# Performance work log

Hardware: AMD Instinct MI355X
Metric: run time of the kernel (lower is better)

## Reference

```python
import jax, jax.numpy as jnp
import numpy as np

H, C, PQ, PV, CZ, CS = 12, 16, 4, 8, 128, 384
W_C = (2.0 / (9.0 * PQ)) ** 0.5
INV_SQRT3 = 3.0 ** -0.5


def setup_inputs() -> dict:
    key = jax.random.key(0)
    ks = jax.random.split(key, 20)
    B, N = 2, 512
    s = jax.random.normal(ks[0], (B, N, CS), jnp.float32)
    z = jax.random.normal(ks[1], (B, N, N, CZ), jnp.float32)
    m = jax.random.normal(ks[2], (B, N, 3, 3), jnp.float32)
    rot, _ = jnp.linalg.qr(m)  # proper-ish rotations (orthonormal frames)
    trans = jax.random.normal(ks[3], (B, N, 3), jnp.float32)
    seq_mask = jnp.ones((B, N), jnp.float32)
    sc = 0.02
    params = {
        'Wq': jax.random.normal(ks[4], (CS, H * C)) * sc,
        'bq': jnp.zeros((H * C,)),
        'Wkv': jax.random.normal(ks[5], (CS, H * C * 2)) * sc,
        'bkv': jnp.zeros((H * C * 2,)),
        'Wb': jax.random.normal(ks[6], (CZ, H)) * sc,
        'bb': jnp.zeros((H,)),
        'Wqp': jax.random.normal(ks[7], (CS, 3 * PQ * H)) * sc,
        'bqp': jnp.zeros((3 * PQ * H,)),
        'Wkvp': jax.random.normal(ks[8], (CS, 3 * (PQ + PV) * H)) * sc,
        'bkvp': jnp.zeros((3 * (PQ + PV) * H,)),
        'gamma': jnp.zeros((H,)),
        'Wout': jax.random.normal(ks[9], ((CZ + C + PV * 4) * H, CS)) * sc,
        'bout': jnp.zeros((CS,)),
    }
    return dict(s=s, z=z, rot=rot, trans=trans, seq_mask=seq_mask, **params)


def reference(s, z, rot, trans, seq_mask, Wq, bq, Wkv, bkv, Wb, bb, Wqp, bqp, Wkvp, bkvp, gamma, Wout, bout):
    B, N, _ = s.shape
    # scalar q/k/v
    q = (s @ Wq + bq).reshape(B, N, H, C)
    kv = (s @ Wkv + bkv).reshape(B, N, H, 2 * C)
    k, v = kv[..., :C], kv[..., C:]
    qp = s @ Wqp + bqp                                   # (B,N,3*PQ*H)
    qp = jnp.stack(jnp.split(qp, 3, axis=-1), axis=-1)   # (B,N,PQ*H,3)
    qp = jnp.einsum('bixy,bipy->bipx', rot, qp) + trans[:, :, None, :]
    qp = qp.reshape(B, N, H, PQ, 3)
    # key/value points
    kvp = s @ Wkvp + bkvp
    kvp = jnp.stack(jnp.split(kvp, 3, axis=-1), axis=-1)  # (B,N,(PQ+PV)*H,3)
    kvp = jnp.einsum('bixy,bipy->bipx', rot, kvp) + trans[:, :, None, :]
    kvp = kvp.reshape(B, N, H, PQ + PV, 3)
    kp, vp = kvp[..., :PQ, :], kvp[..., PQ:, :]
    # attention logits: scalar term + pair bias + point-distance term
    bpair = (z @ Wb + bb).transpose(0, 3, 1, 2)          # (B,H,i,j)
    a = jnp.einsum('bihc,bjhc->bhij', q, k) * (3 * C) ** -0.5 + INV_SQRT3 * bpair
    d2 = jnp.sum((qp[:, :, None] - kp[:, None]) ** 2, axis=-1)   # (B,i,j,H,PQ)
    pa = -0.5 * jnp.sum(d2, axis=-1)                      # (B,i,j,H)
    head_w = jax.nn.softplus(gamma)
    pa = pa * (head_w * W_C * INV_SQRT3)
    a = a + pa.transpose(0, 3, 1, 2)
    mask_bias = 100000.0 * (seq_mask[:, :, None] * seq_mask[:, None, :] - 1.0)
    a = a + mask_bias[:, None, :, :]
    a = jax.nn.softmax(a, axis=-1)                        # (B,H,i,j)
    # outputs: scalar values, rotated points (inverse frame), pair features
    o = jnp.einsum('bhij,bjhc->bihc', a, v).reshape(B, N, H * C)
    op = jnp.einsum('bhij,bjhpx->bihpx', a, vp)           # (B,i,H,PV,3)
    op = jnp.einsum('biyx,bihpy->bihpx', rot, op - trans[:, :, None, None, :])  # R^T(p-t)
    onorm = jnp.maximum(jnp.sqrt(jnp.sum(op ** 2, axis=-1)), 1e-6).reshape(B, N, H * PV)
    op = op.reshape(B, N, H * PV, 3)
    opair = jnp.einsum('bhij,bijc->bihc', a, z).reshape(B, N, H * CZ)
    feat = jnp.concatenate([o, op[..., 0], op[..., 1], op[..., 2], onorm, opair], axis=-1)
    return feat @ Wout + bout
```

## Files before the change

kernel.cpp:

```cpp
#include <hip/hip_runtime.h>
#include <hip/hip_bf16.h>

constexpr int B = 2, N = 512, H = 12, C = 16, PQ = 4, PV = 8, CZ = 128, CS = 384;
constexpr int HC   = H * C;
constexpr int FEAT = (CZ + C + PV * 4) * H;
constexpr float QK_SCALE  = 0.14433756729740643f;
constexpr float INV_SQRT3 = 0.5773502691896258f;
constexpr float WC_IS3    = 0.13608276348795434f;

using f32x4 = __attribute__((ext_vector_type(4))) float;
using s16x8 = __attribute__((ext_vector_type(8))) short;

__device__ __forceinline__ short f2b(float f) {
    union { __hip_bfloat16 b; short s; } u;
    u.b = __float2bfloat16(f);
    return u.s;
}
__device__ __forceinline__ float b2f(short s) {
    union { short s; __hip_bfloat16 b; } u;
    u.s = s;
    return __bfloat162float(u.b);
}

__device__ __forceinline__ size_t kkps_idx(int row, int col) {
    return ((size_t)((row >> 4) * 12 + (col >> 5))) * 512
         + (size_t)(((row & 15) << 2) + ((col & 31) >> 3)) * 8 + (col & 7);
}

constexpr int RPB = 2;

__global__ __launch_bounds__(256) void k_proj(
    const float* __restrict__ s, const float* __restrict__ rot, const float* __restrict__ trans,
    const float* __restrict__ Wq, const float* __restrict__ bq,
    const float* __restrict__ Wkv, const float* __restrict__ bkv,
    const float* __restrict__ Wqp, const float* __restrict__ bqp,
    const float* __restrict__ Wkvp, const float* __restrict__ bkvp,
    const float* __restrict__ gamma, const float* __restrict__ bb,
    const float* __restrict__ Wout,
    short* __restrict__ qcw, short* __restrict__ kkpS,
    float* __restrict__ vw, float* __restrict__ vpw,
    short* __restrict__ pcw, float* __restrict__ auxw,
    short* __restrict__ WT)
{
    __shared__ float s_s[RPB][CS];
    __shared__ float rawqp_s[RPB][144];
    __shared__ float rawkvp_s[RPB][432];
    __shared__ float qrot_s[RPB][48][3];
    __shared__ float sq_s[RPB][48];
    __shared__ float R_s[RPB][9], T_s[RPB][3];
    const int t = threadIdx.x;
    const int bi0 = blockIdx.x * RPB;

    for (int idx = t; idx < RPB * CS / 4; idx += 256) {
        int r = idx / (CS / 4), k4 = idx % (CS / 4);
        ((float4*)s_s[r])[k4] = ((const float4*)(s + (size_t)(bi0 + r) * CS))[k4];
    }
    if (t < RPB * 9) R_s[t / 9][t % 9] = rot[bi0 * 9 + t];
    if (t < RPB * 3) T_s[t / 3][t % 3] = trans[bi0 * 3 + t];
    __syncthreads();

    for (int qd = t; qd < 288; qd += 256) {
        const int c = qd * 4;
        const float* Wp; int ldw; const float* bp;
        int seg;
        if (c < 192)      { Wp = Wq   + c;        ldw = 192; bp = bq + c;        seg = 0; }
        else if (c < 576) { Wp = Wkv  + (c - 192); ldw = 384; bp = bkv + (c - 192); seg = 1; }
        else if (c < 720) { Wp = Wqp  + (c - 576); ldw = 144; bp = bqp + (c - 576); seg = 2; }
        else              { Wp = Wkvp + (c - 720); ldw = 432; bp = bkvp + (c - 720); seg = 3; }
        float4 bv = *(const float4*)bp;
        float acc[RPB][4];
        #pragma unroll
        for (int r = 0; r < RPB; ++r) {
            acc[r][0] = bv.x; acc[r][1] = bv.y; acc[r][2] = bv.z; acc[r][3] = bv.w;
        }
        for (int k4 = 0; k4 < CS / 4; ++k4) {
            float4 sv[RPB];
            #pragma unroll
            for (int r = 0; r < RPB; ++r) sv[r] = *(const float4*)&s_s[r][k4 * 4];
            #pragma unroll
            for (int e = 0; e < 4; ++e) {
                float4 wv = *(const float4*)(Wp + (size_t)(k4 * 4 + e) * ldw);
                #pragma unroll
                for (int r = 0; r < RPB; ++r) {
                    float se = ((const float*)&sv[r])[e];
                    acc[r][0] += se * wv.x; acc[r][1] += se * wv.y;
                    acc[r][2] += se * wv.z; acc[r][3] += se * wv.w;
                }
            }
        }
        if (seg == 0) {
            #pragma unroll
            for (int r = 0; r < RPB; ++r) {
                short4 o = make_short4(f2b(QK_SCALE * acc[r][0]), f2b(QK_SCALE * acc[r][1]),
                                       f2b(QK_SCALE * acc[r][2]), f2b(QK_SCALE * acc[r][3]));
                *(short4*)&qcw[(size_t)(bi0 + r) * 192 + c] = o;
            }
        } else if (seg == 1) {
            int cc = c - 192, h = cc >> 5, w5 = cc & 31;
            if (w5 < 16) {
                int col = h * 16 + w5;
                #pragma unroll
                for (int r = 0; r < RPB; ++r) {
                    short4 o = make_short4(f2b(acc[r][0]), f2b(acc[r][1]),
                                           f2b(acc[r][2]), f2b(acc[r][3]));
                    *(short4*)&kkpS[kkps_idx(bi0 + r, col)] = o;
                }
            } else {
                #pragma unroll
                for (int r = 0; r < RPB; ++r) {
                    int row = bi0 + r;
                    *(float4*)&vw[(size_t)row * 192 + h * 16 + (w5 - 16)] =
                        (float4){acc[r][0], acc[r][1], acc[r][2], acc[r][3]};
                }
            }
        } else if (seg == 2) {
            #pragma unroll
            for (int r = 0; r < RPB; ++r)
                *(float4*)&rawqp_s[r][c - 576] = (float4){acc[r][0], acc[r][1], acc[r][2], acc[r][3]};
        } else {
            #pragma unroll
            for (int r = 0; r < RPB; ++r)
                *(float4*)&rawkvp_s[r][c - 720] = (float4){acc[r][0], acc[r][1], acc[r][2], acc[r][3]};
        }
    }
    __syncthreads();

    for (int idx = t; idx < RPB * 48; idx += 256) {
        int r = idx / 48, p = idx % 48;
        float y0 = rawqp_s[r][p], y1 = rawqp_s[r][48 + p], y2 = rawqp_s[r][96 + p];
        #pragma unroll
        for (int x = 0; x < 3; ++x)
            qrot_s[r][p][x] = T_s[r][x] + R_s[r][x * 3] * y0 + R_s[r][x * 3 + 1] * y1 + R_s[r][x * 3 + 2] * y2;
    }
    for (int idx = t; idx < RPB * 144; idx += 256) {
        int r = idx / 144, p = idx % 144, h = p / 12, pp = p % 12;
        float y0 = rawkvp_s[r][p], y1 = rawkvp_s[r][144 + p], y2 = rawkvp_s[r][288 + p];
        float vals[3]; float ss = 0.0f;
        #pragma unroll
        for (int x = 0; x < 3; ++x) {
            float v = T_s[r][x] + R_s[r][x * 3] * y0 + R_s[r][x * 3 + 1] * y1 + R_s[r][x * 3 + 2] * y2;
            vals[x] = v; ss += v * v;
        }
        int row = bi0 + r;
        if (pp < PQ) {
            #pragma unroll
            for (int x = 0; x < 3; ++x)
                kkpS[kkps_idx(row, 192 + h * 16 + pp * 3 + x)] = f2b(vals[x]);
            sq_s[r][h * 4 + pp] = ss;
        } else {
            #pragma unroll
            for (int x = 0; x < 3; ++x)
                vpw[(size_t)row * 288 + h * 24 + (pp - PQ) * 3 + x] = vals[x];
        }
    }
    __syncthreads();

    if (t < RPB * 12) {
        int r = t / 12, h = t % 12, row = bi0 + r;
        float g = gamma[h];
        float sp = fmaxf(g, 0.0f) + log1pf(expf(-fabsf(g)));
        float pac = -0.5f * sp * WC_IS3;
        float kpsq = sq_s[r][h * 4] + sq_s[r][h * 4 + 1] + sq_s[r][h * 4 + 2] + sq_s[r][h * 4 + 3];
        kkpS[kkps_idx(row, 192 + h * 16 + 12)] = f2b(kpsq);
        kkpS[kkps_idx(row, 192 + h * 16 + 13)] = 0;
        kkpS[kkps_idx(row, 192 + h * 16 + 14)] = 0;
        kkpS[kkps_idx(row, 192 + h * 16 + 15)] = 0;
        float qpsq = 0.0f;
        #pragma unroll
        for (int pq = 0; pq < 4; ++pq)
            #pragma unroll
            for (int x = 0; x < 3; ++x) {
                float qv = qrot_s[r][h * 4 + pq][x];
                qpsq += qv * qv;
                pcw[(size_t)row * 192 + h * 16 + pq * 3 + x] = f2b(-2.0f * pac * qv);
            }
        pcw[(size_t)row * 192 + h * 16 + 12] = f2b(pac);
        pcw[(size_t)row * 192 + h * 16 + 13] = 0;
        pcw[(size_t)row * 192 + h * 16 + 14] = 0;
        pcw[(size_t)row * 192 + h * 16 + 15] = 0;
        auxw[(size_t)row * 16 + h] = INV_SQRT3 * bb[h] + pac * qpsq;
    }
    if (t >= RPB * 12 && t < RPB * 16) {
        int r = (t - RPB * 12) >> 2, hh = 12 + ((t - RPB * 12) & 3);
        auxw[(size_t)(bi0 + r) * 16 + hh] = 0.0f;
    }

    short* tileb = (short*)&s_s[0][0];
    for (int tile = blockIdx.x; tile < 66 * 12; tile += 512) {
        const int k0 = (tile % 66) * 32;
        const int c0 = (tile / 66) * 32;
        __syncthreads();
        {
            int r = t >> 3, c4 = (t & 7) * 4;
            float4 v = *(const float4*)&Wout[(size_t)(k0 + r) * CS + c0 + c4];
            tileb[(c4 + 0) * 33 + r] = f2b(v.x);
            tileb[(c4 + 1) * 33 + r] = f2b(v.y);
            tileb[(c4 + 2) * 33 + r] = f2b(v.z);
            tileb[(c4 + 3) * 33 + r] = f2b(v.w);
        }
        __syncthreads();
        {
            int rr = t >> 3, k4 = (t & 7) * 4;
            short4 o = make_short4(tileb[rr * 33 + k4], tileb[rr * 33 + k4 + 1],
                                   tileb[rr * 33 + k4 + 2], tileb[rr * 33 + k4 + 3]);
            *(short4*)&WT[(size_t)(c0 + rr) * FEAT + k0 + k4] = o;
        }
    }
}

constexpr int PLS = 520;
constexpr int BSEL = 56;

#define LOADZ(BUF, PTR)                                                  \
    {                                                                    \
        _Pragma("unroll")                                                \
        for (int k4 = 0; k4 < 4; ++k4) {                                 \
            BUF[k4 * 2]     = *(const float4*)((PTR) + k4 * 32);         \
            BUF[k4 * 2 + 1] = *(const float4*)((PTR) + k4 * 32 + 4);     \
        }                                                                \
    }

#define COMPUTE(BUF, JC, KPTR)                                                     \
    {                                                                              \
        s16x8 zf[4];                                                               \
        _Pragma("unroll")                                                          \
        for (int kk = 0; kk < 4; ++kk) {                                           \
            float4 u0 = BUF[kk * 2], u1 = BUF[kk * 2 + 1];                         \
            s16x8 f;                                                               \
            f[0] = f2b(u0.x); f[1] = f2b(u0.y); f[2] = f2b(u0.z); f[3] = f2b(u0.w);\
            f[4] = f2b(u1.x); f[5] = f2b(u1.y); f[6] = f2b(u1.z); f[7] = f2b(u1.w);\
            zf[kk] = f;                                                            \
        }                                                                          \
        f32x4 accA = (f32x4){0, 0, 0, 0}, accB = (f32x4){0, 0, 0, 0};              \
        f32x4 accC = (f32x4){0, 0, 0, 0}, accD = (f32x4){0, 0, 0, 0};              \
        _Pragma("unroll")                                                          \
        for (int kk = 0; kk < 4; ++kk) {                                           \
            s16x8 wb = *(const s16x8*)(bl + kk * 8);                               \
            accA = __builtin_amdgcn_mfma_f32_16x16x32_bf16(zf[kk], wb, accA, 0, 0, 0);\
        }                                                                          \
        s16x8 qselr = *(const s16x8*)(bl + 32);                                    \
        s16x8 pselr = *(const s16x8*)(bl + 40);                                    \
        _Pragma("unroll")                                                          \
        for (int kk = 0; kk < 4; ++kk) {                                           \
            s16x8 af = *(const s16x8*)((KPTR) + kk * 512);                         \
            s16x8 bsel = (kk == half) ? qselr : z8;                                \
            accB = __builtin_amdgcn_mfma_f32_16x16x32_bf16(af, bsel, accB, 0, 0, 0); \
        }                                                                          \
        _Pragma("unroll")                                                          \
        for (int kk = 4; kk < 8; ++kk) {                                           \
            s16x8 af = *(const s16x8*)((KPTR) + kk * 512);                         \
            s16x8 bsel;                                                            \
            if (kk < 6) bsel = (kk == half) ? qselr : z8;                          \
            else        bsel = ((kk - 6) == half) ? pselr : z8;                    \
            accC = __builtin_amdgcn_mfma_f32_16x16x32_bf16(af, bsel, accC, 0, 0, 0); \
        }                                                                          \
        _Pragma("unroll")                                                          \
        for (int kk = 8; kk < 12; ++kk) {                                          \
            s16x8 af = *(const s16x8*)((KPTR) + kk * 512);                         \
            s16x8 bsel = ((kk - 6) == half) ? pselr : z8;                          \
            accD = __builtin_amdgcn_mfma_f32_16x16x32_bf16(af, bsel, accD, 0, 0, 0); \
        }                                                                          \
        f32x4 acc = (accA + accB) + (accC + accD);                                 \
        float4 m4 = *(const float4*)(mkp + (JC) * 16);                             \
        float lo[4]; float cm = -INFINITY;                                         \
        _Pragma("unroll")                                                          \
        for (int r = 0; r < 4; ++r) {                                              \
            lo[r] = acc[r] + constH + 100000.0f * (mask_i * ((const float*)&m4)[r] - 1.0f); \
            cm = fmaxf(cm, lo[r]);                                                 \
        }                                                                          \
        cm = fmaxf(cm, __shfl_xor(cm, 16, 64));                                    \
        cm = fmaxf(cm, __shfl_xor(cm, 32, 64));                                    \
        float mnew = fmaxf(m_run, cm);                                             \
        float sc = __expf(m_run - mnew);                                           \
        m_run = mnew;                                                              \
        float p[4]; float ps = 0.0f;                                               \
        _Pragma("unroll")                                                          \
        for (int r = 0; r < 4; ++r) { p[r] = __expf(lo[r] - mnew); ps += p[r]; }   \
        ps += __shfl_xor(ps, 16, 64);                                              \
        ps += __shfl_xor(ps, 32, 64);                                              \
        l_run = l_run * sc + ps;                                                   \
        if (sc != 1.0f) {                                                          \
            for (int jj = lg * 4; jj < (JC) * 16; jj += 16) {                      \
                short* pr = &P_lds[m15 * PLS + jw + jj];                           \
                _Pragma("unroll")                                                  \
                for (int r = 0; r < 4; ++r) pr[r] = f2b(b2f(pr[r]) * sc);          \
            }                                                                      \
        }                                                                          \
        *(short4*)&P_lds[m15 * PLS + jw + (JC) * 16 + lg * 4] =                    \
            make_short4(f2b(p[0]), f2b(p[1]), f2b(p[2]), f2b(p[3]));               \
    }

__global__ __launch_bounds__(256) void k_attn2(
    const float* __restrict__ z, const float* __restrict__ rot, const float* __restrict__ trans,
    const float* __restrict__ seq_mask,
    const float* __restrict__ Wb,
    const short* __restrict__ qcw, const short* __restrict__ kkpS,
    const short* __restrict__ pcw, const float* __restrict__ auxw,
    const float* __restrict__ vw, const float* __restrict__ vpw,
    short* __restrict__ featb)
{
    __shared__ short P_lds[16 * PLS];
    __shared__ __align__(16) char ovl[7680];
    short* bsel_lds = (short*)ovl;
    float* ored_s   = (float*)ovl;
    float* opred_s  = (float*)(ovl + 3072);
    float* op_f     = (float*)(ovl + 6528);
    __shared__ float ml_s[4][16], ll_s[4][16], M_s[16], Linv_s[16];
    __shared__ float R_s[9], T_s[3];

    const int t = threadIdx.x;
    const int w   = t >> 6;
    const int l   = t & 63;
    const int lg  = l >> 4;
    const int m15 = l & 15;
    const int bi  = blockIdx.x;
    const int b   = bi >> 9;
    const int i   = bi & (N - 1);

    if (t < 9) R_s[t] = rot[bi * 9 + t];
    if (t < 3) T_s[t] = trans[bi * 3 + t];

    const bool hv = (m15 < 12);
    const int hcl = hv ? m15 : 0;
    const int half = m15 >> 1;
    const float constH = auxw[(size_t)bi * 16 + m15];
    const float mask_i = seq_mask[bi];

    if (w == 0) {
        short* dst = &bsel_lds[l * BSEL];
        #pragma unroll
        for (int kk = 0; kk < 4; ++kk)
            #pragma unroll
            for (int e = 0; e < 8; ++e) {
                int c = kk * 32 + lg * 8 + e;
                dst[kk * 8 + e] = f2b(hv ? INV_SQRT3 * Wb[c * H + hcl] : 0.0f);
            }
        const bool selh = ((lg >> 1) == (m15 & 1));
        const s16x8 z8v = {0, 0, 0, 0, 0, 0, 0, 0};
        const short* qrow = qcw + (size_t)bi * 192 + hcl * 16;
        s16x8 qlo = *(const s16x8*)qrow;
        s16x8 qhi = *(const s16x8*)(qrow + 8);
        s16x8 q = (hv && selh) ? ((lg & 1) ? qhi : qlo) : z8v;
        const short* prow = pcw + (size_t)bi * 192 + hcl * 16;
        s16x8 plo = *(const s16x8*)prow;
        s16x8 phi = *(const s16x8*)(prow + 8);
        s16x8 p = (hv && selh) ? ((lg & 1) ? phi : plo) : z8v;
        *(s16x8*)(dst + 32) = q;
        *(s16x8*)(dst + 40) = p;
    }
    __syncthreads();

    float m_run = -INFINITY, l_run = 0.0f;

    const size_t zbase = ((size_t)b * N + i) * (size_t)(N * CZ);
    const int jw = w * 128;
    const float* zAp = z + zbase + (size_t)(jw + m15) * CZ + lg * 8;
    const short* kAp = kkpS + ((size_t)(b * 32 + (jw >> 4))) * 6144
                            + (size_t)(m15 * 4 + lg) * 8;
    const float* mkp = seq_mask + b * N + jw + lg * 4;
    const short* bl = &bsel_lds[l * BSEL];
    const s16x8 z8 = {0, 0, 0, 0, 0, 0, 0, 0};

    float4 bufA[8], bufB[8];
    LOADZ(bufA, zAp);

    for (int jc2 = 0; jc2 < 8; jc2 += 2) {
        LOADZ(bufB, zAp + 16 * CZ);
        COMPUTE(bufA, jc2, kAp);
        kAp += 6144;
        {
            const float* nx = zAp + ((jc2 == 6) ? (16 * CZ) : (32 * CZ));
            LOADZ(bufA, nx);
        }
        COMPUTE(bufB, jc2 + 1, kAp);
        kAp += 6144;
        zAp += 32 * CZ;
    }

    if (lg == 0) { ml_s[w][m15] = m_run; ll_s[w][m15] = l_run; }
    __syncthreads();
    if (t < 16) {
        float M = ml_s[0][t];
        M = fmaxf(M, ml_s[1][t]); M = fmaxf(M, ml_s[2][t]); M = fmaxf(M, ml_s[3][t]);
        float Lt = 0.0f;
        #pragma unroll
        for (int ww = 0; ww < 4; ++ww) Lt += ll_s[ww][t] * __expf(ml_s[ww][t] - M);
        M_s[t] = M;
        Linv_s[t] = 1.0f / Lt;
    }
    __syncthreads();

    {
        const int h = t >> 4, j0t = (t & 15) * 32;
        const int wv = j0t >> 7;
        const float sS = __expf(ml_s[wv][h] - M_s[h]) * Linv_s[h];
        #pragma unroll
        for (int k = 0; k < 4; ++k) {
            s16x8 v = *(const s16x8*)&P_lds[h * PLS + j0t + k * 8];
            s16x8 o;
            #pragma unroll
            for (int e = 0; e < 8; ++e) o[e] = f2b(b2f(v[e]) * sS);
            *(s16x8*)&P_lds[h * PLS + j0t + k * 8] = o;
        }
    }
    __syncthreads();

    short* F = featb + (size_t)bi * FEAT;

    f32x4 oa0 = (f32x4){0, 0, 0, 0}, oa1 = (f32x4){0, 0, 0, 0};
    const int c0 = w * 32;
    #pragma unroll 4
    for (int kk = 0; kk < 16; ++kk) {
        s16x8 af = *(const s16x8*)&P_lds[m15 * PLS + kk * 32 + lg * 8];
        const float* zb = z + zbase + (size_t)(kk * 32 + lg * 8) * CZ + c0 + m15;
        s16x8 b0f, b1f;
        #pragma unroll
        for (int e = 0; e < 8; ++e) {
            b0f[e] = f2b(zb[(size_t)e * CZ]);
            b1f[e] = f2b(zb[(size_t)e * CZ + 16]);
        }
        oa0 = __builtin_amdgcn_mfma_f32_16x16x32_bf16(af, b0f, oa0, 0, 0, 0);
        oa1 = __builtin_amdgcn_mfma_f32_16x16x32_bf16(af, b1f, oa1, 0, 0, 0);
    }
    #pragma unroll
    for (int r = 0; r < 4; ++r) {
        int h = lg * 4 + r;
        if (h < 12) {
            F[576 + h * 128 + c0 + m15]      = f2b(oa0[r]);
            F[576 + h * 128 + c0 + 16 + m15] = f2b(oa1[r]);
        }
    }

    if (t < 192) {
        const int c4 = t % 48, jg = t / 48;
        const int h = c4 >> 2;
        const short* Pr = &P_lds[h * PLS + jg * 128];
        const float* vb = vw + ((size_t)b * N + jg * 128) * 192 + c4 * 4;
        f32x4 a = (f32x4){0, 0, 0, 0};
        #pragma unroll 2
        for (int q = 0; q < 16; ++q) {
            s16x8 pv = *(const s16x8*)(Pr + q * 8);
            #pragma unroll
            for (int e = 0; e < 8; ++e) {
                float4 v4 = *(const float4*)(vb + (size_t)(q * 8 + e) * 192);
                float pj = b2f(pv[e]);
                a[0] += pj * v4.x; a[1] += pj * v4.y; a[2] += pj * v4.z; a[3] += pj * v4.w;
            }
        }
        *(f32x4*)&ored_s[jg * 192 + c4 * 4] = a;
    }

    if (t < 216) {
        const int c4 = t % 72, jg = t / 72;
        const int h = c4 / 6;
        const int j0g = (jg == 0) ? 0 : (jg == 1 ? 176 : 352);
        const int nq = (jg == 2) ? 20 : 22;
        const short* Pr = &P_lds[h * PLS + j0g];
        const float* vb = vpw + ((size_t)b * N + j0g) * 288 + c4 * 4;
        f32x4 a = (f32x4){0, 0, 0, 0};
        #pragma unroll 2
        for (int q = 0; q < nq; ++q) {
            s16x8 pv = *(const s16x8*)(Pr + q * 8);
            #pragma unroll
            for (int e = 0; e < 8; ++e) {
                float4 v4 = *(const float4*)(vb + (size_t)(q * 8 + e) * 288);
                float pj = b2f(pv[e]);
                a[0] += pj * v4.x; a[1] += pj * v4.y; a[2] += pj * v4.z; a[3] += pj * v4.w;
            }
        }
        *(f32x4*)&opred_s[jg * 288 + c4 * 4] = a;
    }
    __syncthreads();

    if (t < 192)
        F[t] = f2b(ored_s[t] + ored_s[192 + t] + ored_s[384 + t] + ored_s[576 + t]);
    if (t < 72) {
        #pragma unroll
        for (int x = 0; x < 4; ++x) {
            int rv = t * 4 + x;
            op_f[rv] = opred_s[rv] + opred_s[288 + rv] + opred_s[576 + rv];
        }
    }
    __syncthreads();

    if (t < 96) {
        float o0 = op_f[t * 3 + 0] - T_s[0];
        float o1 = op_f[t * 3 + 1] - T_s[1];
        float o2 = op_f[t * 3 + 2] - T_s[2];
        float n2 = 0.0f;
        #pragma unroll
        for (int x = 0; x < 3; ++x) {
            float rx = R_s[0 * 3 + x] * o0 + R_s[1 * 3 + x] * o1 + R_s[2 * 3 + x] * o2;
            F[HC + 96 * x + t] = f2b(rx);
            n2 += rx * rx;
        }
        F[480 + t] = f2b(fmaxf(sqrtf(n2), 1e-6f));
    }
}

__global__ __launch_bounds__(256) void k_out(
    const short* __restrict__ featb, const short* __restrict__ WT,
    const float* __restrict__ bout, float* __restrict__ out)
{
    __shared__ short A_s[32 * 40];
    __shared__ short B_s[32 * 40];
    const int t = threadIdx.x;
    const int w   = t >> 6;
    const int l   = t & 63;
    const int lg  = l >> 4;
    const int m15 = l & 15;
    const int wm = w >> 1, wn = w & 1;
    const int bm = (blockIdx.x / 12) * 32;
    const int bn = (blockIdx.x % 12) * 32;

    f32x4 acc = (f32x4){0, 0, 0, 0};

    const int sr = (t & 127) >> 2;
    const int sk = (t & 3) * 8;

    s16x8 rS;
    if (t < 128) rS = *(const s16x8*)&featb[(size_t)(bm + sr) * FEAT + sk];
    else         rS = *(const s16x8*)&WT[(size_t)(bn + sr) * FEAT + sk];

    for (int k0 = 0; k0 < FEAT; k0 += 32) {
        __syncthreads();
        if (t < 128) *(s16x8*)&A_s[sr * 40 + sk] = rS;
        else         *(s16x8*)&B_s[sr * 40 + sk] = rS;
        __syncthreads();

        const int kn = k0 + 32;
        if (kn < FEAT) {
            if (t < 128) rS = *(const s16x8*)&featb[(size_t)(bm + sr) * FEAT + kn + sk];
            else         rS = *(const s16x8*)&WT[(size_t)(bn + sr) * FEAT + kn + sk];
        }

        s16x8 af = *(const s16x8*)&A_s[(wm * 16 + m15) * 40 + lg * 8];
        s16x8 bf = *(const s16x8*)&B_s[(wn * 16 + m15) * 40 + lg * 8];
        acc = __builtin_amdgcn_mfma_f32_16x16x32_bf16(af, bf, acc, 0, 0, 0);
    }

    {
        int col = bn + wn * 16 + m15;
        float bo = bout[col];
        #pragma unroll
        for (int r = 0; r < 4; ++r) {
            int row = bm + wm * 16 + lg * 4 + r;
            out[(size_t)row * CS + col] = acc[r] + bo;
        }
    }
}

extern "C" void kernel_launch(void* const* d_in, const int* in_sizes, int n_in,
                              void* d_out, int out_size, void* d_ws, size_t ws_size,
                              hipStream_t stream)
{
    const float* s     = (const float*)d_in[0];
    const float* z     = (const float*)d_in[1];
    const float* rot   = (const float*)d_in[2];
    const float* trans = (const float*)d_in[3];
    const float* mask  = (const float*)d_in[4];
    const float* Wq    = (const float*)d_in[5];
    const float* bq    = (const float*)d_in[6];
    const float* Wkv   = (const float*)d_in[7];
    const float* bkv   = (const float*)d_in[8];
    const float* Wb    = (const float*)d_in[9];
    const float* bb    = (const float*)d_in[10];
    const float* Wqp   = (const float*)d_in[11];
    const float* bqp   = (const float*)d_in[12];
    const float* Wkvp  = (const float*)d_in[13];
    const float* bkvp  = (const float*)d_in[14];
    const float* gamma = (const float*)d_in[15];
    const float* Wout  = (const float*)d_in[16];
    const float* bout  = (const float*)d_in[17];

    char* wsb = (char*)d_ws;
    short* featb = (short*)wsb;
    float* vw    = (float*)(wsb + 4325376);
    float* vpw   = (float*)(wsb + 5111808);
    float* auxw  = (float*)(wsb + 6291456);
    short* qcw   = (short*)(wsb + 6356992);
    short* pcw   = (short*)(wsb + 6750208);
    short* kkpS  = (short*)(wsb + 7143424);
    short* WT    = (short*)(wsb + 7929856);

    hipLaunchKernelGGL(k_proj, dim3(B * N / RPB), dim3(256), 0, stream,
                       s, rot, trans, Wq, bq, Wkv, bkv, Wqp, bqp, Wkvp, bkvp,
                       gamma, bb, Wout, qcw, kkpS, vw, vpw, pcw, auxw, WT);
    hipLaunchKernelGGL(k_attn2, dim3(B * N), dim3(256), 0, stream,
                       z, rot, trans, mask, Wb, qcw, kkpS, pcw, auxw, vw, vpw, featb);
    hipLaunchKernelGGL(k_out, dim3(384), dim3(256), 0, stream,
                       featb, WT, bout, (float*)d_out);
}
```

Before: 258.3 us.

## Split attention key range across two blocks per row with merge kernel

Each query row's 512 keys are now processed by two blocks of 256 keys each. Each block writes unnormalized partial outputs plus its softmax max and sum to a workspace buffer. A new merge kernel rescales and combines the partials, then applies the inverse frame rotation and norm. This doubles block-level parallelism and halves per-block serial work and LDS footprint, at the cost of an extra kernel launch and a global round trip of about 16 KB of partials per row.

```diff
diff --git a/kernel.cpp b/kernel.cpp
--- a/kernel.cpp
+++ b/kernel.cpp
@@ -208,7 +208,7 @@
     }
 }
 
-constexpr int PLS = 520;
+constexpr int PLS2 = 264;
 constexpr int BSEL = 56;
 
 #define LOADZ(BUF, PTR)                                                  \
@@ -281,50 +281,48 @@
         l_run = l_run * sc + ps;                                                   \
         if (sc != 1.0f) {                                                          \
             for (int jj = lg * 4; jj < (JC) * 16; jj += 16) {                      \
-                short* pr = &P_lds[m15 * PLS + jw + jj];                           \
+                short* pr = &P_lds[m15 * PLS2 + jwl + jj];                         \
                 _Pragma("unroll")                                                  \
                 for (int r = 0; r < 4; ++r) pr[r] = f2b(b2f(pr[r]) * sc);          \
             }                                                                      \
         }                                                                          \
-        *(short4*)&P_lds[m15 * PLS + jw + (JC) * 16 + lg * 4] =                    \
+        *(short4*)&P_lds[m15 * PLS2 + jwl + (JC) * 16 + lg * 4] =                  \
             make_short4(f2b(p[0]), f2b(p[1]), f2b(p[2]), f2b(p[3]));               \
     }
 
-__global__ __launch_bounds__(256) void k_attn2(
-    const float* __restrict__ z, const float* __restrict__ rot, const float* __restrict__ trans,
-    const float* __restrict__ seq_mask,
+__global__ __launch_bounds__(256) void k_attn2s(
+    const float* __restrict__ z, const float* __restrict__ seq_mask,
     const float* __restrict__ Wb,
     const short* __restrict__ qcw, const short* __restrict__ kkpS,
     const short* __restrict__ pcw, const float* __restrict__ auxw,
     const float* __restrict__ vw, const float* __restrict__ vpw,
-    short* __restrict__ featb)
+    float* __restrict__ part)
 {
-    __shared__ short P_lds[16 * PLS];
+    __shared__ short P_lds[16 * PLS2];
     __shared__ __align__(16) char ovl[7680];
     short* bsel_lds = (short*)ovl;
     float* ored_s   = (float*)ovl;
     float* opred_s  = (float*)(ovl + 3072);
-    float* op_f     = (float*)(ovl + 6528);
-    __shared__ float ml_s[4][16], ll_s[4][16], M_s[16], Linv_s[16];
-    __shared__ float R_s[9], T_s[3];
+    __shared__ float ml_s[4][16], ll_s[4][16], M_s[16];
 
     const int t = threadIdx.x;
     const int w   = t >> 6;
     const int l   = t & 63;
     const int lg  = l >> 4;
     const int m15 = l & 15;
-    const int bi  = blockIdx.x;
+    const int bi    = blockIdx.x >> 1;
+    const int half2 = blockIdx.x & 1;
+    const int jbase = half2 << 8;
     const int b   = bi >> 9;
     const int i   = bi & (N - 1);
-
-    if (t < 9) R_s[t] = rot[bi * 9 + t];
-    if (t < 3) T_s[t] = trans[bi * 3 + t];
 
     const bool hv = (m15 < 12);
     const int hcl = hv ? m15 : 0;
     const int half = m15 >> 1;
     const float constH = auxw[(size_t)bi * 16 + m15];
     const float mask_i = seq_mask[bi];
+
+    float* myp = part + (size_t)blockIdx.x * 2048;
 
     if (w == 0) {
         short* dst = &bsel_lds[l * BSEL];
@@ -353,7 +351,8 @@
     float m_run = -INFINITY, l_run = 0.0f;
 
     const size_t zbase = ((size_t)b * N + i) * (size_t)(N * CZ);
-    const int jw = w * 128;
+    const int jw  = jbase + w * 64;
+    const int jwl = w * 64;
     const float* zAp = z + zbase + (size_t)(jw + m15) * CZ + lg * 8;
     const short* kAp = kkpS + ((size_t)(b * 32 + (jw >> 4))) * 6144
                             + (size_t)(m15 * 4 + lg) * 8;
@@ -364,12 +363,12 @@
     float4 bufA[8], bufB[8];
     LOADZ(bufA, zAp);
 
-    for (int jc2 = 0; jc2 < 8; jc2 += 2) {
+    for (int jc2 = 0; jc2 < 4; jc2 += 2) {
         LOADZ(bufB, zAp + 16 * CZ);
         COMPUTE(bufA, jc2, kAp);
         kAp += 6144;
         {
-            const float* nx = zAp + ((jc2 == 6) ? (16 * CZ) : (32 * CZ));
+            const float* nx = zAp + ((jc2 == 2) ? (16 * CZ) : (32 * CZ));
             LOADZ(bufA, nx);
         }
         COMPUTE(bufB, jc2 + 1, kAp);
@@ -386,33 +385,32 @@
         #pragma unroll
         for (int ww = 0; ww < 4; ++ww) Lt += ll_s[ww][t] * __expf(ml_s[ww][t] - M);
         M_s[t] = M;
-        Linv_s[t] = 1.0f / Lt;
+        myp[t] = M;
+        myp[16 + t] = Lt;
     }
     __syncthreads();
 
     {
-        const int h = t >> 4, j0t = (t & 15) * 32;
-        const int wv = j0t >> 7;
-        const float sS = __expf(ml_s[wv][h] - M_s[h]) * Linv_s[h];
-        #pragma unroll
-        for (int k = 0; k < 4; ++k) {
-            s16x8 v = *(const s16x8*)&P_lds[h * PLS + j0t + k * 8];
+        const int h = t >> 4, j0t = (t & 15) * 16;
+        const int wv = j0t >> 6;
+        const float sS = __expf(ml_s[wv][h] - M_s[h]);
+        #pragma unroll
+        for (int k = 0; k < 2; ++k) {
+            s16x8 v = *(const s16x8*)&P_lds[h * PLS2 + j0t + k * 8];
             s16x8 o;
             #pragma unroll
             for (int e = 0; e < 8; ++e) o[e] = f2b(b2f(v[e]) * sS);
-            *(s16x8*)&P_lds[h * PLS + j0t + k * 8] = o;
-        }
-    }
-    __syncthreads();
-
-    short* F = featb + (size_t)bi * FEAT;
+            *(s16x8*)&P_lds[h * PLS2 + j0t + k * 8] = o;
+        }
+    }
+    __syncthreads();
 
     f32x4 oa0 = (f32x4){0, 0, 0, 0}, oa1 = (f32x4){0, 0, 0, 0};
     const int c0 = w * 32;
     #pragma unroll 4
-    for (int kk = 0; kk < 16; ++kk) {
-        s16x8 af = *(const s16x8*)&P_lds[m15 * PLS + kk * 32 + lg * 8];
-        const float* zb = z + zbase + (size_t)(kk * 32 + lg * 8) * CZ + c0 + m15;
+    for (int kk = 0; kk < 8; ++kk) {
+        s16x8 af = *(const s16x8*)&P_lds[m15 * PLS2 + kk * 32 + lg * 8];
+        const float* zb = z + zbase + (size_t)(jbase + kk * 32 + lg * 8) * CZ + c0 + m15;
         s16x8 b0f, b1f;
         #pragma unroll
         for (int e = 0; e < 8; ++e) {
@@ -426,19 +424,19 @@
     for (int r = 0; r < 4; ++r) {
         int h = lg * 4 + r;
         if (h < 12) {
-            F[576 + h * 128 + c0 + m15]      = f2b(oa0[r]);
-            F[576 + h * 128 + c0 + 16 + m15] = f2b(oa1[r]);
+            myp[32 + h * 128 + c0 + m15]      = oa0[r];
+            myp[32 + h * 128 + c0 + 16 + m15] = oa1[r];
         }
     }
 
     if (t < 192) {
         const int c4 = t % 48, jg = t / 48;
         const int h = c4 >> 2;
-        const short* Pr = &P_lds[h * PLS + jg * 128];
-        const float* vb = vw + ((size_t)b * N + jg * 128) * 192 + c4 * 4;
+        const short* Pr = &P_lds[h * PLS2 + jg * 64];
+        const float* vb = vw + ((size_t)b * N + jbase + jg * 64) * 192 + c4 * 4;
         f32x4 a = (f32x4){0, 0, 0, 0};
         #pragma unroll 2
-        for (int q = 0; q < 16; ++q) {
+        for (int q = 0; q < 8; ++q) {
             s16x8 pv = *(const s16x8*)(Pr + q * 8);
             #pragma unroll
             for (int e = 0; e < 8; ++e) {
@@ -450,16 +448,14 @@
         *(f32x4*)&ored_s[jg * 192 + c4 * 4] = a;
     }
 
-    if (t < 216) {
+    if (t < 144) {
         const int c4 = t % 72, jg = t / 72;
         const int h = c4 / 6;
-        const int j0g = (jg == 0) ? 0 : (jg == 1 ? 176 : 352);
-        const int nq = (jg == 2) ? 20 : 22;
-        const short* Pr = &P_lds[h * PLS + j0g];
-        const float* vb = vpw + ((size_t)b * N + j0g) * 288 + c4 * 4;
+        const short* Pr = &P_lds[h * PLS2 + jg * 128];
+        const float* vb = vpw + ((size_t)b * N + jbase + jg * 128) * 288 + c4 * 4;
         f32x4 a = (f32x4){0, 0, 0, 0};
         #pragma unroll 2
-        for (int q = 0; q < nq; ++q) {
+        for (int q = 0; q < 16; ++q) {
             s16x8 pv = *(const s16x8*)(Pr + q * 8);
             #pragma unroll
             for (int e = 0; e < 8; ++e) {
@@ -473,12 +469,54 @@
     __syncthreads();
 
     if (t < 192)
-        F[t] = f2b(ored_s[t] + ored_s[192 + t] + ored_s[384 + t] + ored_s[576 + t]);
-    if (t < 72) {
-        #pragma unroll
-        for (int x = 0; x < 4; ++x) {
-            int rv = t * 4 + x;
-            op_f[rv] = opred_s[rv] + opred_s[288 + rv] + opred_s[576 + rv];
+        myp[1568 + t] = ored_s[t] + ored_s[192 + t] + ored_s[384 + t] + ored_s[576 + t];
+    #pragma unroll
+    for (int rep = 0; rep < 2; ++rep) {
+        int rv = t + rep * 256;
+        if (rv < 288) myp[1760 + rv] = opred_s[rv] + opred_s[288 + rv];
+    }
+}
+
+__global__ __launch_bounds__(256) void k_mrg(
+    const float* __restrict__ part, const float* __restrict__ rot, const float* __restrict__ trans,
+    short* __restrict__ featb)
+{
+    __shared__ float s0_s[16], s1_s[16], op_f[288];
+    __shared__ float R_s[9], T_s[3];
+    const int t = threadIdx.x;
+    const int bi = blockIdx.x;
+    const float* p0 = part + (size_t)bi * 4096;
+    const float* p1 = p0 + 2048;
+
+    if (t < 9) R_s[t] = rot[bi * 9 + t];
+    if (t < 3) T_s[t] = trans[bi * 3 + t];
+    if (t < 12) {
+        float m0 = p0[t], l0 = p0[16 + t];
+        float m1 = p1[t], l1 = p1[16 + t];
+        float M = fmaxf(m0, m1);
+        float e0 = __expf(m0 - M), e1 = __expf(m1 - M);
+        float Li = 1.0f / (l0 * e0 + l1 * e1);
+        s0_s[t] = e0 * Li;
+        s1_s[t] = e1 * Li;
+    }
+    __syncthreads();
+
+    short* F = featb + (size_t)bi * FEAT;
+    #pragma unroll
+    for (int r = 0; r < 6; ++r) {
+        int v = t + 256 * r; int h = v >> 7;
+        F[576 + v] = f2b(p0[32 + v] * s0_s[h] + p1[32 + v] * s1_s[h]);
+    }
+    if (t < 192) {
+        int h = t >> 4;
+        F[t] = f2b(p0[1568 + t] * s0_s[h] + p1[1568 + t] * s1_s[h]);
+    }
+    #pragma unroll
+    for (int rep = 0; rep < 2; ++rep) {
+        int rv = t + rep * 256;
+        if (rv < 288) {
+            int h = rv / 24;
+            op_f[rv] = p0[1760 + rv] * s0_s[h] + p1[1760 + rv] * s1_s[h];
         }
     }
     __syncthreads();
@@ -582,12 +620,15 @@
     short* pcw   = (short*)(wsb + 6750208);
     short* kkpS  = (short*)(wsb + 7143424);
     short* WT    = (short*)(wsb + 7929856);
+    float* partw = (float*)(wsb + 9551872);
 
     hipLaunchKernelGGL(k_proj, dim3(B * N / RPB), dim3(256), 0, stream,
                        s, rot, trans, Wq, bq, Wkv, bkv, Wqp, bqp, Wkvp, bkvp,
                        gamma, bb, Wout, qcw, kkpS, vw, vpw, pcw, auxw, WT);
-    hipLaunchKernelGGL(k_attn2, dim3(B * N), dim3(256), 0, stream,
-                       z, rot, trans, mask, Wb, qcw, kkpS, pcw, auxw, vw, vpw, featb);
+    hipLaunchKernelGGL(k_attn2s, dim3(B * N * 2), dim3(256), 0, stream,
+                       z, mask, Wb, qcw, kkpS, pcw, auxw, vw, vpw, partw);
+    hipLaunchKernelGGL(k_mrg, dim3(B * N), dim3(256), 0, stream,
+                       partw, rot, trans, featb);
     hipLaunchKernelGGL(k_out, dim3(384), dim3(256), 0, stream,
                        featb, WT, bout, (float*)d_out);
 }
```

Result: slower. 273.5 us (+5.9%).

## Store per-chunk softmax maxima instead of rescaling P history; prefetch K fragments

Applied to the files above, without the earlier changes.

The online softmax no longer rescales previously written probabilities in LDS whenever the running maximum changes. Each 16-column chunk is now exponentiated against its own local max, which is saved to a small shared array, and the final normalization pass applies a per-chunk correction factor. K-side MFMA operands for the query-point part are also software-prefetched one chunk ahead alongside the z loads, and the accumulators are merged from four into two. This removes the data-dependent LDS read-modify-write loop but adds register pressure from the prefetched fragments and an extra exp per normalization step.

```diff
diff --git a/kernel.cpp b/kernel.cpp
--- a/kernel.cpp
+++ b/kernel.cpp
@@ -220,47 +220,42 @@
         }                                                                \
     }
 
-#define COMPUTE(BUF, JC, KPTR)                                                     \
+#define LOADK6(KF, PTR)                                                  \
+    {                                                                    \
+        _Pragma("unroll")                                                \
+        for (int kk = 0; kk < 6; ++kk)                                   \
+            KF[kk] = *(const s16x8*)((PTR) + kk * 512);                  \
+    }
+
+#define COMPUTE(BUF, KPRE, KPTR, JC)                                               \
     {                                                                              \
-        s16x8 zf[4];                                                               \
+        s16x8 k6[6];                                                               \
+        _Pragma("unroll")                                                          \
+        for (int kk = 0; kk < 6; ++kk)                                             \
+            k6[kk] = *(const s16x8*)((KPTR) + (6 + kk) * 512);                     \
+        f32x4 accA = (f32x4){0, 0, 0, 0}, accB = (f32x4){0, 0, 0, 0};              \
         _Pragma("unroll")                                                          \
         for (int kk = 0; kk < 4; ++kk) {                                           \
             float4 u0 = BUF[kk * 2], u1 = BUF[kk * 2 + 1];                         \
             s16x8 f;                                                               \
             f[0] = f2b(u0.x); f[1] = f2b(u0.y); f[2] = f2b(u0.z); f[3] = f2b(u0.w);\
             f[4] = f2b(u1.x); f[5] = f2b(u1.y); f[6] = f2b(u1.z); f[7] = f2b(u1.w);\
-            zf[kk] = f;                                                            \
-        }                                                                          \
-        f32x4 accA = (f32x4){0, 0, 0, 0}, accB = (f32x4){0, 0, 0, 0};              \
-        f32x4 accC = (f32x4){0, 0, 0, 0}, accD = (f32x4){0, 0, 0, 0};              \
-        _Pragma("unroll")                                                          \
-        for (int kk = 0; kk < 4; ++kk) {                                           \
             s16x8 wb = *(const s16x8*)(bl + kk * 8);                               \
-            accA = __builtin_amdgcn_mfma_f32_16x16x32_bf16(zf[kk], wb, accA, 0, 0, 0);\
+            accA = __builtin_amdgcn_mfma_f32_16x16x32_bf16(f, wb, accA, 0, 0, 0);  \
         }                                                                          \
         s16x8 qselr = *(const s16x8*)(bl + 32);                                    \
         s16x8 pselr = *(const s16x8*)(bl + 40);                                    \
         _Pragma("unroll")                                                          \
-        for (int kk = 0; kk < 4; ++kk) {                                           \
-            s16x8 af = *(const s16x8*)((KPTR) + kk * 512);                         \
+        for (int kk = 0; kk < 6; ++kk) {                                           \
             s16x8 bsel = (kk == half) ? qselr : z8;                                \
-            accB = __builtin_amdgcn_mfma_f32_16x16x32_bf16(af, bsel, accB, 0, 0, 0); \
+            accB = __builtin_amdgcn_mfma_f32_16x16x32_bf16(KPRE[kk], bsel, accB, 0, 0, 0); \
         }                                                                          \
         _Pragma("unroll")                                                          \
-        for (int kk = 4; kk < 8; ++kk) {                                           \
-            s16x8 af = *(const s16x8*)((KPTR) + kk * 512);                         \
-            s16x8 bsel;                                                            \
-            if (kk < 6) bsel = (kk == half) ? qselr : z8;                          \
-            else        bsel = ((kk - 6) == half) ? pselr : z8;                    \
-            accC = __builtin_amdgcn_mfma_f32_16x16x32_bf16(af, bsel, accC, 0, 0, 0); \
+        for (int kk = 0; kk < 6; ++kk) {                                           \
+            s16x8 bsel = (kk == half) ? pselr : z8;                                \
+            accA = __builtin_amdgcn_mfma_f32_16x16x32_bf16(k6[kk], bsel, accA, 0, 0, 0); \
         }                                                                          \
-        _Pragma("unroll")                                                          \
-        for (int kk = 8; kk < 12; ++kk) {                                          \
-            s16x8 af = *(const s16x8*)((KPTR) + kk * 512);                         \
-            s16x8 bsel = ((kk - 6) == half) ? pselr : z8;                          \
-            accD = __builtin_amdgcn_mfma_f32_16x16x32_bf16(af, bsel, accD, 0, 0, 0); \
-        }                                                                          \
-        f32x4 acc = (accA + accB) + (accC + accD);                                 \
+        f32x4 acc = accA + accB;                                                   \
         float4 m4 = *(const float4*)(mkp + (JC) * 16);                             \
         float lo[4]; float cm = -INFINITY;                                         \
         _Pragma("unroll")                                                          \
@@ -270,22 +265,16 @@
         }                                                                          \
         cm = fmaxf(cm, __shfl_xor(cm, 16, 64));                                    \
         cm = fmaxf(cm, __shfl_xor(cm, 32, 64));                                    \
+        float p[4]; float ps = 0.0f;                                               \
+        _Pragma("unroll")                                                          \
+        for (int r = 0; r < 4; ++r) { p[r] = __expf(lo[r] - cm); ps += p[r]; }     \
+        ps += __shfl_xor(ps, 16, 64);                                              \
+        ps += __shfl_xor(ps, 32, 64);                                              \
         float mnew = fmaxf(m_run, cm);                                             \
         float sc = __expf(m_run - mnew);                                           \
+        l_run = l_run * sc + ps * __expf(cm - mnew);                               \
         m_run = mnew;                                                              \
-        float p[4]; float ps = 0.0f;                                               \
-        _Pragma("unroll")                                                          \
-        for (int r = 0; r < 4; ++r) { p[r] = __expf(lo[r] - mnew); ps += p[r]; }   \
-        ps += __shfl_xor(ps, 16, 64);                                              \
-        ps += __shfl_xor(ps, 32, 64);                                              \
-        l_run = l_run * sc + ps;                                                   \
-        if (sc != 1.0f) {                                                          \
-            for (int jj = lg * 4; jj < (JC) * 16; jj += 16) {                      \
-                short* pr = &P_lds[m15 * PLS + jw + jj];                           \
-                _Pragma("unroll")                                                  \
-                for (int r = 0; r < 4; ++r) pr[r] = f2b(b2f(pr[r]) * sc);          \
-            }                                                                      \
-        }                                                                          \
+        if (lg == 0) mc_s[w][m15][JC] = cm;                                        \
         *(short4*)&P_lds[m15 * PLS + jw + (JC) * 16 + lg * 4] =                    \
             make_short4(f2b(p[0]), f2b(p[1]), f2b(p[2]), f2b(p[3]));               \
     }
@@ -306,6 +295,7 @@
     float* opred_s  = (float*)(ovl + 3072);
     float* op_f     = (float*)(ovl + 6528);
     __shared__ float ml_s[4][16], ll_s[4][16], M_s[16], Linv_s[16];
+    __shared__ float mc_s[4][16][8];
     __shared__ float R_s[9], T_s[3];
 
     const int t = threadIdx.x;
@@ -362,19 +352,23 @@
     const s16x8 z8 = {0, 0, 0, 0, 0, 0, 0, 0};
 
     float4 bufA[8], bufB[8];
+    s16x8 kpA[6], kpB[6];
     LOADZ(bufA, zAp);
+    LOADK6(kpA, kAp);
 
     for (int jc2 = 0; jc2 < 8; jc2 += 2) {
         LOADZ(bufB, zAp + 16 * CZ);
-        COMPUTE(bufA, jc2, kAp);
-        kAp += 6144;
+        LOADK6(kpB, kAp + 6144);
+        COMPUTE(bufA, kpA, kAp, jc2);
         {
-            const float* nx = zAp + ((jc2 == 6) ? (16 * CZ) : (32 * CZ));
-            LOADZ(bufA, nx);
-        }
-        COMPUTE(bufB, jc2 + 1, kAp);
-        kAp += 6144;
+            const float* nz = zAp + ((jc2 == 6) ? (16 * CZ) : (32 * CZ));
+            const short* nk = kAp + ((jc2 == 6) ? 6144 : 12288);
+            LOADZ(bufA, nz);
+            LOADK6(kpA, nk);
+        }
+        COMPUTE(bufB, kpB, kAp + 6144, jc2 + 1);
         zAp += 32 * CZ;
+        kAp += 12288;
     }
 
     if (lg == 0) { ml_s[w][m15] = m_run; ll_s[w][m15] = l_run; }
@@ -393,9 +387,11 @@
     {
         const int h = t >> 4, j0t = (t & 15) * 32;
         const int wv = j0t >> 7;
-        const float sS = __expf(ml_s[wv][h] - M_s[h]) * Linv_s[h];
+        const float Li = Linv_s[h], Mh = M_s[h];
         #pragma unroll
         for (int k = 0; k < 4; ++k) {
+            const int lc = ((j0t & 127) >> 4) + (k >> 1);
+            const float sS = __expf(mc_s[wv][h][lc] - Mh) * Li;
             s16x8 v = *(const s16x8*)&P_lds[h * PLS + j0t + k * 8];
             s16x8 o;
             #pragma unroll
```

Result: no change. 258.8 us (+0.2%).
